# Optimization experiments

Hardware: AMD Instinct MI355X
Metric: run time of the kernel (lower is better)

## Reference

```python
import jax, jax.numpy as jnp
import numpy as np

B, P, OBS = 65536, 3, 48      # batch, players, per-player obs dim
N_PROP, N_EXT = 9, 2          # 9 prop encoders, players-1 = 2 teammate encoders
TEAM_OPP = 18 + 6 * N_EXT     # = 30; opponent slice starts here
OPP = OBS - TEAM_OPP          # = 18
ACT_DIM = 3
EXT_OUT = 576 // N_EXT        # = 288
ACT_LIMIT = 1.0
NEG_SLOPE = 0.01              # torch LeakyReLU default


def setup_inputs() -> dict:
    key = jax.random.key(0)
    ks = iter(jax.random.split(key, 32))
    r = lambda shape: jax.random.normal(next(ks), shape, jnp.float32) * 0.05
    return {
        "obs": jax.random.normal(next(ks), (B, P, OBS), jnp.float32),
        # 9 propEncoders per player: [2 -> 32 -> 64]
        "prop_W1": r((P, N_PROP, 2, 32)),  "prop_b1": r((P, N_PROP, 32)),
        "prop_W2": r((P, N_PROP, 32, 64)), "prop_b2": r((P, N_PROP, 64)),
        # 2 extEncoders per player: [6 -> 32 -> 288]
        "ext_W1": r((P, N_EXT, 6, 32)),       "ext_b1": r((P, N_EXT, 32)),
        "ext_W2": r((P, N_EXT, 32, EXT_OUT)), "ext_b2": r((P, N_EXT, EXT_OUT)),
        # oppEncoder per player: [18 -> 32 -> 576]
        "opp_W1": r((P, OPP, 32)),  "opp_b1": r((P, 32)),
        "opp_W2": r((P, 32, 576)),  "opp_b2": r((P, 576)),
        # pi head per player: [576 -> 256 -> 256 -> act_dim], LeakyReLU, Tanh out
        "pi_W1": r((P, 576, 256)),     "pi_b1": r((P, 256)),
        "pi_W2": r((P, 256, 256)),     "pi_b2": r((P, 256)),
        "pi_W3": r((P, 256, ACT_DIM)), "pi_b3": r((P, ACT_DIM)),
    }


def reference(obs, prop_W1, prop_b1, prop_W2, prop_b2,
              ext_W1, ext_b1, ext_W2, ext_b2,
              opp_W1, opp_b1, opp_W2, opp_b2,
              pi_W1, pi_b1, pi_W2, pi_b2, pi_W3, pi_b3):
    lrelu = lambda x: jax.nn.leaky_relu(x, NEG_SLOPE)
    b = obs.shape[0]

    # --- prop encoders: 9 tiny MLPs on 2-wide slices, batched via einsum ---
    o_prop = obs[:, :, :2 * N_PROP].reshape(b, P, N_PROP, 2)
    h = lrelu(jnp.einsum('bpni,pnio->bpno', o_prop, prop_W1) + prop_b1)
    h = lrelu(jnp.einsum('bpni,pnio->bpno', h, prop_W2) + prop_b2)  # [B,P,9,64]
    enc = h.reshape(b, P, 9 * 64)  # concat over the 9 encoders -> [B,P,576]

    # --- ext encoders: n_players-1 MLPs on 6-wide slices ---
    o_ext = obs[:, :, 18:TEAM_OPP].reshape(b, P, N_EXT, 6)
    e = lrelu(jnp.einsum('bpni,pnio->bpno', o_ext, ext_W1) + ext_b1)
    e = lrelu(jnp.einsum('bpni,pnio->bpno', e, ext_W2) + ext_b2)    # [B,P,2,288]
    enc = enc + e.reshape(b, P, 576)

    # --- opp encoder on the remaining slice ---
    o_opp = obs[:, :, TEAM_OPP:]
    z = lrelu(jnp.einsum('bpi,pio->bpo', o_opp, opp_W1) + opp_b1)
    z = lrelu(jnp.einsum('bpi,pio->bpo', z, opp_W2) + opp_b2)       # [B,P,576]
    enc = enc + z

    # --- actor head: 576 -> 256 -> 256 -> act_dim, tanh * act_limit ---
    h1 = lrelu(jnp.einsum('bpi,pio->bpo', enc, pi_W1) + pi_b1)
    h2 = lrelu(jnp.einsum('bpi,pio->bpo', h1, pi_W2) + pi_b2)
    out = jnp.tanh(jnp.einsum('bpi,pio->bpo', h2, pi_W3) + pi_b3)
    return ACT_LIMIT * out  # [B, P, act_dim]
```

## Files before the change

kernel.cpp:

```cpp
#include <hip/hip_runtime.h>
#include <math.h>


#define NEG_SLOPE 0.01f

#define OFF_B1A  0
#define OFF_ENCB 9216
#define OFF_PW1  175104
#define OFF_PW2  617472
#define OFF_PW3  814080
#define WS_TOTAL 826368

#define TILE_ENCB 18
#define TILE_PW1  342
#define TILE_PW2  1206
#define TILE_PW3  1590
#define TILE_END  1614

#define OBS_STRIDE 48
#define HS_STRIDE  104
#define ENC_STRIDE 200
#define H_STRIDE   264

typedef short bf16x8 __attribute__((ext_vector_type(8)));
typedef float f32x4  __attribute__((ext_vector_type(4)));
typedef float f32x2  __attribute__((ext_vector_type(2)));

__device__ __forceinline__ float lrelu(float x) { return fmaxf(x, NEG_SLOPE * x); }

__device__ __forceinline__ float u2f(unsigned int u) {
  union { unsigned int u; float f; } c; c.u = u; return c.f;
}

__device__ __forceinline__ unsigned int pk2bf(float a, float b) {
  union { float f; unsigned int u; } ca, cb; ca.f = a; cb.f = b;
  return __builtin_amdgcn_perm(cb.u + 0x8000u, ca.u + 0x8000u, 0x07060302u);
}

__device__ __forceinline__ unsigned short f2bf(float x) {
  union { float f; unsigned int u; } c; c.f = x;
  unsigned int u = (c.u + 0x7fffu + ((c.u >> 16) & 1u)) >> 16;
  return (unsigned short)u;
}

__global__ __launch_bounds__(256) void prep_kernel(
    const float* __restrict__ propW2, const float* __restrict__ extW1,
    const float* __restrict__ extW2,  const float* __restrict__ oppW1,
    const float* __restrict__ oppW2,  const float* __restrict__ piW1,
    const float* __restrict__ piW2,   const float* __restrict__ piW3,
    unsigned short* __restrict__ ws16)
{
  const int u = blockIdx.x * 256 + threadIdx.x;
  if (u >= (WS_TOTAL >> 3)) return;
  const int lane = u & 63;
  const int t = u >> 6;
  const int lm = lane & 15;
  const int kbase = (lane >> 4) << 3;

  unsigned short o8[8];

  if (t < TILE_ENCB) {
    int s = t;
    const int nt2 = s & 1; s >>= 1;
    const int go = s % 3; const int p = s / 3;
    const int n = go * 32 + nt2 * 16 + lm;
    #pragma unroll
    for (int j = 0; j < 8; ++j) {
      const int d = 16 + kbase + j;
      float v;
      if (n < 64) {
        const int g = n >> 5, o = n & 31, i = d - 18 - 6 * g;
        v = (i >= 0 && i < 6) ? extW1[((p * 2 + g) * 6 + i) * 32 + o] : 0.f;
      } else {
        const int o = n - 64, i = d - 30;
        v = (i >= 0) ? oppW1[(p * 18 + i) * 32 + o] : 0.f;
      }
      o8[j] = f2bf(v);
    }
  } else if (t < TILE_PW1) {
    int s = t - TILE_ENCB;
    const int nt2 = s & 1; s >>= 1;
    const int br = s % 3; s /= 3;
    const int kt = s % 18; const int p = s / 18;
    const int n = kt * 32 + nt2 * 16 + lm;
    #pragma unroll
    for (int j = 0; j < 8; ++j) {
      const int k_pos = kbase + j;
      const int kperm = (k_pos & 1) * 16 + (k_pos >> 1);
      float v;
      if (br == 0)      { const int g = kt >> 1;   v = propW2[((p*9+g)*32 + k_pos)*64 + (n - g*64)]; }
      else if (br == 1) { const int g = (kt >= 9); v = extW2 [((p*2+g)*32 + kperm)*288 + (n - g*288)]; }
      else              {                          v = oppW2 [(p*32 + kperm)*576 + n]; }
      o8[j] = f2bf(v);
    }
  } else if (t < TILE_PW2) {
    int s = t - TILE_PW1;
    const int nt = s & 15; s >>= 4;
    const int kt = s % 18; const int p = s / 18;
    const int col = nt * 16 + lm;
    #pragma unroll
    for (int j = 0; j < 8; ++j) {
      const int k_pos = kbase + j;
      const int kperm = (k_pos & 1) * 16 + (k_pos >> 1);
      o8[j] = f2bf(piW1[(p * 576 + kt * 32 + kperm) * 256 + col]);
    }
  } else if (t < TILE_PW3) {
    int s = t - TILE_PW2;
    const int nt = s & 15; s >>= 4;
    const int kt = s & 7; const int p = s >> 3;
    const int col = nt * 16 + lm;
    #pragma unroll
    for (int j = 0; j < 8; ++j) {
      const int k_pos = kbase + j;
      const int kperm = (k_pos & 1) * 16 + (k_pos >> 1);
      o8[j] = f2bf(piW2[(p * 256 + kt * 32 + kperm) * 256 + col]);
    }
  } else {
    int s = t - TILE_PW3;
    const int kt = s & 7; const int p = s >> 3;
    #pragma unroll
    for (int j = 0; j < 8; ++j) {
      const int k_pos = kbase + j;
      const int kperm = (k_pos & 1) * 16 + (k_pos >> 1);
      o8[j] = (lm < 3) ? f2bf(piW3[(p * 256 + kt * 32 + kperm) * 3 + lm]) : (unsigned short)0;
    }
  }

  *(uint4*)&ws16[(size_t)u * 8] = *(const uint4*)o8;
}

__global__ __launch_bounds__(256, 3) void fused_kernel(
    const float* __restrict__ obs,
    const float* __restrict__ propW1, const float* __restrict__ propB1,
    const float* __restrict__ propB2,
    const float* __restrict__ extB1,  const float* __restrict__ extB2,
    const float* __restrict__ oppB1,  const float* __restrict__ oppB2,
    const unsigned short* __restrict__ wsAll,
    const float* __restrict__ b1v, const float* __restrict__ b2v,
    const float* __restrict__ b3v,
    float* __restrict__ out)
{
  __shared__ __align__(16) unsigned short obs_s[64 * OBS_STRIDE];
  __shared__ __align__(16) unsigned short Hs[64 * HS_STRIDE];
  __shared__ __align__(16) unsigned short hbuf[64 * H_STRIDE];

  const unsigned short* b1aW = wsAll + OFF_B1A;
  const unsigned short* encB = wsAll + OFF_ENCB;
  const unsigned short* w1sw = wsAll + OFF_PW1;
  const unsigned short* w2sw = wsAll + OFF_PW2;
  const unsigned short* w3sw = wsAll + OFF_PW3;

  const int tid = threadIdx.x;
  const int p = blockIdx.y, brow = blockIdx.x;
  const int sbase = brow * 64;
  const int wv = tid >> 6, l = tid & 63, lm = l & 15, q = l >> 4;
  const f32x4 zz = {0.f, 0.f, 0.f, 0.f};

  {
    const int s = tid >> 2, c4 = tid & 3;
    if (c4 < 3) {
      const int c0 = c4 * 16;
      const float4* src = (const float4*)&obs[(sbase + s) * 144 + p * 48 + c0];
      float4 v0 = src[0], v1 = src[1], v2 = src[2], v3 = src[3];
      unsigned int pk[8];
      pk[0] = pk2bf(v0.x, v0.y); pk[1] = pk2bf(v0.z, v0.w);
      pk[2] = pk2bf(v1.x, v1.y); pk[3] = pk2bf(v1.z, v1.w);
      pk[4] = pk2bf(v2.x, v2.y); pk[5] = pk2bf(v2.z, v2.w);
      pk[6] = pk2bf(v3.x, v3.y); pk[7] = pk2bf(v3.z, v3.w);
      *(uint4*)&obs_s[s * OBS_STRIDE + c0]     = *(uint4*)&pk[0];
      *(uint4*)&obs_s[s * OBS_STRIDE + c0 + 8] = *(uint4*)&pk[4];
    }
  }
  __syncthreads();

  if (wv >= 1) {
    const int go = wv - 1;
    bf16x8 af[4];
    #pragma unroll
    for (int ms = 0; ms < 4; ++ms)
      af[ms] = *(const bf16x8*)&obs_s[(ms * 16 + lm) * OBS_STRIDE + 16 + q * 8];
    bf16x8 bf0 = *(const bf16x8*)&b1aW[((p * 3 + go) * 2 + 0) * 512 + l * 8];
    bf16x8 bf1 = *(const bf16x8*)&b1aW[((p * 3 + go) * 2 + 1) * 512 + l * 8];
    float bias0, bias1;
    if (go < 2) { bias0 = extB1[(p*2+go)*32 + lm]; bias1 = extB1[(p*2+go)*32 + 16 + lm]; }
    else        { bias0 = oppB1[p*32 + lm];        bias1 = oppB1[p*32 + 16 + lm]; }
    const f32x4 cb0 = {bias0, bias0, bias0, bias0};
    const f32x4 cb1 = {bias1, bias1, bias1, bias1};
    #pragma unroll
    for (int ms = 0; ms < 4; ++ms) {
      f32x4 c0 = __builtin_amdgcn_mfma_f32_16x16x32_bf16(af[ms], bf0, cb0, 0, 0, 0);
      f32x4 c1 = __builtin_amdgcn_mfma_f32_16x16x32_bf16(af[ms], bf1, cb1, 0, 0, 0);
      #pragma unroll
      for (int r = 0; r < 4; ++r) {
        unsigned int w = pk2bf(lrelu(c0[r]), lrelu(c1[r]));
        *(unsigned int*)&Hs[(ms * 16 + q * 4 + r) * HS_STRIDE + go * 32 + lm * 2] = w;
      }
    }
  }
  __syncthreads();

  float b1r[4];
  #pragma unroll
  for (int nt = 0; nt < 4; ++nt) b1r[nt] = b1v[p * 256 + wv * 64 + nt * 16 + lm];
  f32x4 acc[4][4];
  #pragma unroll
  for (int a = 0; a < 4; ++a)
    #pragma unroll
    for (int b = 0; b < 4; ++b) {
      f32x4 cb = {b1r[b], b1r[b], b1r[b], b1r[b]};
      acc[a][b] = cb;
    }

  for (int g = 0; g < 3; ++g) {
    int kts[2]; int nkt = 1;
    kts[0] = g * 6 + wv;
    if ((g & 1) == 0 && wv < 2)       { kts[1] = g * 6 + 4 + wv;       nkt = 2; }
    else if ((g & 1) == 1 && wv >= 2) { kts[1] = g * 6 + 4 + (wv - 2); nkt = 2; }

    for (int ik = 0; ik < nkt; ++ik) {
      const int kt = kts[ik], ktloc = kt - g * 6;
      const int gp = kt >> 1, ge = (kt >= 9) ? 1 : 0;

      bf16x8 apf[4];
      {
        f32x2 w0v[4], w1v[4], bbv[4];
        const float4* p4 = (const float4*)&propW1[(p * 9 + gp) * 64];
        float4 t0a = p4[q * 2],     t0b = p4[q * 2 + 1];
        float4 t1a = p4[8 + q * 2], t1b = p4[8 + q * 2 + 1];
        const float4* pb4 = (const float4*)&propB1[(p * 9 + gp) * 32];
        float4 tba = pb4[q * 2],    tbb = pb4[q * 2 + 1];
        w0v[0] = (f32x2){t0a.x, t0a.y}; w0v[1] = (f32x2){t0a.z, t0a.w};
        w0v[2] = (f32x2){t0b.x, t0b.y}; w0v[3] = (f32x2){t0b.z, t0b.w};
        w1v[0] = (f32x2){t1a.x, t1a.y}; w1v[1] = (f32x2){t1a.z, t1a.w};
        w1v[2] = (f32x2){t1b.x, t1b.y}; w1v[3] = (f32x2){t1b.z, t1b.w};
        bbv[0] = (f32x2){tba.x, tba.y}; bbv[1] = (f32x2){tba.z, tba.w};
        bbv[2] = (f32x2){tbb.x, tbb.y}; bbv[3] = (f32x2){tbb.z, tbb.w};
        #pragma unroll
        for (int ms = 0; ms < 4; ++ms) {
          const int row = ms * 16 + lm;
          const unsigned int xu = *(const unsigned int*)&obs_s[row * OBS_STRIDE + 2 * gp];
          const f32x2 x0v = {u2f(xu << 16), u2f(xu << 16)};
          const f32x2 x1v = {u2f(xu & 0xffff0000u), u2f(xu & 0xffff0000u)};
          unsigned int au[4];
          #pragma unroll
          for (int jj = 0; jj < 4; ++jj) {
            f32x2 h = bbv[jj] + x0v * w0v[jj] + x1v * w1v[jj];
            h = __builtin_elementwise_max(h, h * NEG_SLOPE);
            au[jj] = pk2bf(h.x, h.y);
          }
          __builtin_memcpy(&apf[ms], au, 16);
        }
      }

      const int ebase = (p * 18 + kt) * 6;
      bf16x8 wpf[2], wef[2], wof[2];
      float bp[2], be[2], bo[2];
      #pragma unroll
      for (int nt2 = 0; nt2 < 2; ++nt2) {
        wpf[nt2] = *(const bf16x8*)&encB[(ebase + nt2) * 512 + l * 8];
        wef[nt2] = *(const bf16x8*)&encB[(ebase + 2 + nt2) * 512 + l * 8];
        wof[nt2] = *(const bf16x8*)&encB[(ebase + 4 + nt2) * 512 + l * 8];
        const int nc = nt2 * 16 + lm;
        bp[nt2] = propB2[(p * 9 + gp) * 64 + (kt & 1) * 32 + nc];
        be[nt2] = extB2[(p * 2 + ge) * 288 + (kt - ge * 9) * 32 + nc];
        bo[nt2] = oppB2[p * 576 + kt * 32 + nc];
      }

      #pragma unroll
      for (int ms = 0; ms < 4; ++ms) {
        const int row = ms * 16 + lm;
        bf16x8 ae = *(const bf16x8*)&Hs[row * HS_STRIDE + ge * 32 + q * 8];
        bf16x8 ao = *(const bf16x8*)&Hs[row * HS_STRIDE + 64 + q * 8];
        float v0[4], v1[4];
        {
          f32x4 cp = __builtin_amdgcn_mfma_f32_16x16x32_bf16(apf[ms], wpf[0], zz, 0, 0, 0);
          f32x4 ce = __builtin_amdgcn_mfma_f32_16x16x32_bf16(ae,      wef[0], zz, 0, 0, 0);
          f32x4 co = __builtin_amdgcn_mfma_f32_16x16x32_bf16(ao,      wof[0], zz, 0, 0, 0);
          #pragma unroll
          for (int r = 0; r < 4; ++r)
            v0[r] = lrelu(cp[r] + bp[0]) + lrelu(ce[r] + be[0]) + lrelu(co[r] + bo[0]);
        }
        {
          f32x4 cp = __builtin_amdgcn_mfma_f32_16x16x32_bf16(apf[ms], wpf[1], zz, 0, 0, 0);
          f32x4 ce = __builtin_amdgcn_mfma_f32_16x16x32_bf16(ae,      wef[1], zz, 0, 0, 0);
          f32x4 co = __builtin_amdgcn_mfma_f32_16x16x32_bf16(ao,      wof[1], zz, 0, 0, 0);
          #pragma unroll
          for (int r = 0; r < 4; ++r)
            v1[r] = lrelu(cp[r] + bp[1]) + lrelu(ce[r] + be[1]) + lrelu(co[r] + bo[1]);
        }
        #pragma unroll
        for (int r = 0; r < 4; ++r)
          *(unsigned int*)&hbuf[(ms * 16 + q * 4 + r) * ENC_STRIDE + ktloc * 32 + lm * 2] =
              pk2bf(v0[r], v1[r]);
      }
    }
    __syncthreads();

    for (int ktloc = 0; ktloc < 6; ++ktloc) {
      const int kt = g * 6 + ktloc;
      bf16x8 afr[4], bfr[4];
      #pragma unroll
      for (int ms = 0; ms < 4; ++ms)
        afr[ms] = *(const bf16x8*)&hbuf[(ms * 16 + lm) * ENC_STRIDE + ktloc * 32 + q * 8];
      const int wb = ((p * 18 + kt) * 16 + wv * 4) * 512 + l * 8;
      #pragma unroll
      for (int nt = 0; nt < 4; ++nt)
        bfr[nt] = *(const bf16x8*)&w1sw[wb + nt * 512];
      #pragma unroll
      for (int ms = 0; ms < 4; ++ms)
        #pragma unroll
        for (int nt = 0; nt < 4; ++nt)
          acc[ms][nt] = __builtin_amdgcn_mfma_f32_16x16x32_bf16(afr[ms], bfr[nt], acc[ms][nt], 0, 0, 0);
    }
    __syncthreads();
  }

  #pragma unroll
  for (int ms = 0; ms < 4; ++ms)
    #pragma unroll
    for (int pi2 = 0; pi2 < 2; ++pi2)
      #pragma unroll
      for (int r = 0; r < 4; ++r) {
        float v0 = lrelu(acc[ms][pi2 * 2][r]);
        float v1 = lrelu(acc[ms][pi2 * 2 + 1][r]);
        *(unsigned int*)&hbuf[(ms * 16 + q * 4 + r) * H_STRIDE + (wv * 2 + pi2) * 32 + lm * 2] =
            pk2bf(v0, v1);
      }
  __syncthreads();

  {
    float b2r[4];
    #pragma unroll
    for (int nt = 0; nt < 4; ++nt) b2r[nt] = b2v[p * 256 + wv * 64 + nt * 16 + lm];
    #pragma unroll
    for (int a = 0; a < 4; ++a)
      #pragma unroll
      for (int b = 0; b < 4; ++b) {
        f32x4 cb = {b2r[b], b2r[b], b2r[b], b2r[b]};
        acc[a][b] = cb;
      }
  }
  for (int kt = 0; kt < 8; ++kt) {
    bf16x8 afr[4], bfr[4];
    #pragma unroll
    for (int ms = 0; ms < 4; ++ms)
      afr[ms] = *(const bf16x8*)&hbuf[(ms * 16 + lm) * H_STRIDE + kt * 32 + q * 8];
    const int wb = ((p * 8 + kt) * 16 + wv * 4) * 512 + l * 8;
    #pragma unroll
    for (int nt = 0; nt < 4; ++nt)
      bfr[nt] = *(const bf16x8*)&w2sw[wb + nt * 512];
    #pragma unroll
    for (int ms = 0; ms < 4; ++ms)
      #pragma unroll
      for (int nt = 0; nt < 4; ++nt)
        acc[ms][nt] = __builtin_amdgcn_mfma_f32_16x16x32_bf16(afr[ms], bfr[nt], acc[ms][nt], 0, 0, 0);
  }
  __syncthreads();
  #pragma unroll
  for (int ms = 0; ms < 4; ++ms)
    #pragma unroll
    for (int pi2 = 0; pi2 < 2; ++pi2)
      #pragma unroll
      for (int r = 0; r < 4; ++r) {
        float v0 = lrelu(acc[ms][pi2 * 2][r]);
        float v1 = lrelu(acc[ms][pi2 * 2 + 1][r]);
        *(unsigned int*)&hbuf[(ms * 16 + q * 4 + r) * H_STRIDE + (wv * 2 + pi2) * 32 + lm * 2] =
            pk2bf(v0, v1);
      }
  __syncthreads();

  const float bias3 = (lm < 3) ? b3v[p * 3 + lm] : 0.f;
  f32x4 a3 = {bias3, bias3, bias3, bias3};
  for (int kt = 0; kt < 8; ++kt) {
    bf16x8 afr = *(const bf16x8*)&hbuf[(wv * 16 + lm) * H_STRIDE + kt * 32 + q * 8];
    bf16x8 bfr = *(const bf16x8*)&w3sw[((p * 8 + kt) * 64 + l) * 8];
    a3 = __builtin_amdgcn_mfma_f32_16x16x32_bf16(afr, bfr, a3, 0, 0, 0);
  }
  if (lm < 3) {
    #pragma unroll
    for (int r = 0; r < 4; ++r) {
      const int s = wv * 16 + q * 4 + r;
      out[(sbase + s) * 9 + p * 3 + lm] = tanhf(a3[r]);
    }
  }
}

extern "C" void kernel_launch(void* const* d_in, const int* in_sizes, int n_in,
                              void* d_out, int out_size, void* d_ws, size_t ws_size,
                              hipStream_t stream)
{
  (void)in_sizes; (void)n_in; (void)out_size; (void)ws_size;
  const float* obs    = (const float*)d_in[0];
  const float* propW1 = (const float*)d_in[1];
  const float* propB1 = (const float*)d_in[2];
  const float* propW2 = (const float*)d_in[3];
  const float* propB2 = (const float*)d_in[4];
  const float* extW1  = (const float*)d_in[5];
  const float* extB1  = (const float*)d_in[6];
  const float* extW2  = (const float*)d_in[7];
  const float* extB2  = (const float*)d_in[8];
  const float* oppW1  = (const float*)d_in[9];
  const float* oppB1  = (const float*)d_in[10];
  const float* oppW2  = (const float*)d_in[11];
  const float* oppB2  = (const float*)d_in[12];
  const float* piW1   = (const float*)d_in[13];
  const float* piB1   = (const float*)d_in[14];
  const float* piW2   = (const float*)d_in[15];
  const float* piB2   = (const float*)d_in[16];
  const float* piW3   = (const float*)d_in[17];
  const float* piB3   = (const float*)d_in[18];
  float* out = (float*)d_out;
  unsigned short* ws16 = (unsigned short*)d_ws;

  prep_kernel<<<dim3(((WS_TOTAL >> 3) + 255) / 256), dim3(256), 0, stream>>>(
      propW2, extW1, extW2, oppW1, oppW2, piW1, piW2, piW3, ws16);

  fused_kernel<<<dim3(65536 / 64, 3), dim3(256), 0, stream>>>(
      obs, propW1, propB1, propB2, extB1, extB2, oppB1, oppB2,
      ws16, piB1, piB2, piB3, out);
}
```

Measured before the change: 245.9 us.

## Double threads per block to eight waves splitting GEMM N-tiles

```diff
diff --git a/kernel.cpp b/kernel.cpp
--- a/kernel.cpp
+++ b/kernel.cpp
@@ -15,7 +15,6 @@
 #define TILE_PW1  342
 #define TILE_PW2  1206
 #define TILE_PW3  1590
-#define TILE_END  1614
 
 #define OBS_STRIDE 48
 #define HS_STRIDE  104
@@ -27,6 +26,11 @@
 typedef float f32x2  __attribute__((ext_vector_type(2)));
 
 __device__ __forceinline__ float lrelu(float x) { return fmaxf(x, NEG_SLOPE * x); }
+
+__device__ __forceinline__ f32x4 lrelu4(f32x4 x) {
+  return __builtin_elementwise_max(x, x * NEG_SLOPE);
+}
+__device__ __forceinline__ f32x4 splat4(float b) { return (f32x4){b, b, b, b}; }
 
 __device__ __forceinline__ float u2f(unsigned int u) {
   union { unsigned int u; float f; } c; c.u = u; return c.f;
@@ -129,7 +133,7 @@
   *(uint4*)&ws16[(size_t)u * 8] = *(const uint4*)o8;
 }
 
-__global__ __launch_bounds__(256, 3) void fused_kernel(
+__global__ __launch_bounds__(512, 6) void fused_kernel(
     const float* __restrict__ obs,
     const float* __restrict__ propW1, const float* __restrict__ propB1,
     const float* __restrict__ propB2,
@@ -156,7 +160,7 @@
   const int wv = tid >> 6, l = tid & 63, lm = l & 15, q = l >> 4;
   const f32x4 zz = {0.f, 0.f, 0.f, 0.f};
 
-  {
+  if (tid < 256) {
     const int s = tid >> 2, c4 = tid & 3;
     if (c4 < 3) {
       const int c0 = c4 * 16;
@@ -173,7 +177,7 @@
   }
   __syncthreads();
 
-  if (wv >= 1) {
+  if (wv >= 1 && wv <= 3) {
     const int go = wv - 1;
     bf16x8 af[4];
     #pragma unroll
@@ -184,41 +188,32 @@
     float bias0, bias1;
     if (go < 2) { bias0 = extB1[(p*2+go)*32 + lm]; bias1 = extB1[(p*2+go)*32 + 16 + lm]; }
     else        { bias0 = oppB1[p*32 + lm];        bias1 = oppB1[p*32 + 16 + lm]; }
-    const f32x4 cb0 = {bias0, bias0, bias0, bias0};
-    const f32x4 cb1 = {bias1, bias1, bias1, bias1};
+    const f32x4 cb0 = splat4(bias0), cb1 = splat4(bias1);
     #pragma unroll
     for (int ms = 0; ms < 4; ++ms) {
-      f32x4 c0 = __builtin_amdgcn_mfma_f32_16x16x32_bf16(af[ms], bf0, cb0, 0, 0, 0);
-      f32x4 c1 = __builtin_amdgcn_mfma_f32_16x16x32_bf16(af[ms], bf1, cb1, 0, 0, 0);
-      #pragma unroll
-      for (int r = 0; r < 4; ++r) {
-        unsigned int w = pk2bf(lrelu(c0[r]), lrelu(c1[r]));
-        *(unsigned int*)&Hs[(ms * 16 + q * 4 + r) * HS_STRIDE + go * 32 + lm * 2] = w;
-      }
+      f32x4 c0 = lrelu4(__builtin_amdgcn_mfma_f32_16x16x32_bf16(af[ms], bf0, cb0, 0, 0, 0));
+      f32x4 c1 = lrelu4(__builtin_amdgcn_mfma_f32_16x16x32_bf16(af[ms], bf1, cb1, 0, 0, 0));
+      #pragma unroll
+      for (int r = 0; r < 4; ++r)
+        *(unsigned int*)&Hs[(ms * 16 + q * 4 + r) * HS_STRIDE + go * 32 + lm * 2] =
+            pk2bf(c0[r], c1[r]);
     }
   }
   __syncthreads();
 
-  float b1r[4];
+  float b1r[2];
   #pragma unroll
-  for (int nt = 0; nt < 4; ++nt) b1r[nt] = b1v[p * 256 + wv * 64 + nt * 16 + lm];
-  f32x4 acc[4][4];
+  for (int nt = 0; nt < 2; ++nt) b1r[nt] = b1v[p * 256 + wv * 32 + nt * 16 + lm];
+  f32x4 acc[4][2];
   #pragma unroll
-  for (int a = 0; a < 4; ++a)
-    #pragma unroll
-    for (int b = 0; b < 4; ++b) {
-      f32x4 cb = {b1r[b], b1r[b], b1r[b], b1r[b]};
-      acc[a][b] = cb;
-    }
+  for (int a = 0; a < 4; ++a) {
+    acc[a][0] = splat4(b1r[0]);
+    acc[a][1] = splat4(b1r[1]);
+  }
 
   for (int g = 0; g < 3; ++g) {
-    int kts[2]; int nkt = 1;
-    kts[0] = g * 6 + wv;
-    if ((g & 1) == 0 && wv < 2)       { kts[1] = g * 6 + 4 + wv;       nkt = 2; }
-    else if ((g & 1) == 1 && wv >= 2) { kts[1] = g * 6 + 4 + (wv - 2); nkt = 2; }
-
-    for (int ik = 0; ik < nkt; ++ik) {
-      const int kt = kts[ik], ktloc = kt - g * 6;
+    if (wv < 6) {
+      const int kt = g * 6 + wv, ktloc = wv;
       const int gp = kt >> 1, ge = (kt >= 9) ? 1 : 0;
 
       bf16x8 apf[4];
@@ -271,116 +266,105 @@
         const int row = ms * 16 + lm;
         bf16x8 ae = *(const bf16x8*)&Hs[row * HS_STRIDE + ge * 32 + q * 8];
         bf16x8 ao = *(const bf16x8*)&Hs[row * HS_STRIDE + 64 + q * 8];
-        float v0[4], v1[4];
+        f32x4 s0, s1;
         {
           f32x4 cp = __builtin_amdgcn_mfma_f32_16x16x32_bf16(apf[ms], wpf[0], zz, 0, 0, 0);
           f32x4 ce = __builtin_amdgcn_mfma_f32_16x16x32_bf16(ae,      wef[0], zz, 0, 0, 0);
           f32x4 co = __builtin_amdgcn_mfma_f32_16x16x32_bf16(ao,      wof[0], zz, 0, 0, 0);
-          #pragma unroll
-          for (int r = 0; r < 4; ++r)
-            v0[r] = lrelu(cp[r] + bp[0]) + lrelu(ce[r] + be[0]) + lrelu(co[r] + bo[0]);
+          s0 = lrelu4(cp + splat4(bp[0])) + lrelu4(ce + splat4(be[0])) + lrelu4(co + splat4(bo[0]));
         }
         {
           f32x4 cp = __builtin_amdgcn_mfma_f32_16x16x32_bf16(apf[ms], wpf[1], zz, 0, 0, 0);
           f32x4 ce = __builtin_amdgcn_mfma_f32_16x16x32_bf16(ae,      wef[1], zz, 0, 0, 0);
           f32x4 co = __builtin_amdgcn_mfma_f32_16x16x32_bf16(ao,      wof[1], zz, 0, 0, 0);
-          #pragma unroll
-          for (int r = 0; r < 4; ++r)
-            v1[r] = lrelu(cp[r] + bp[1]) + lrelu(ce[r] + be[1]) + lrelu(co[r] + bo[1]);
+          s1 = lrelu4(cp + splat4(bp[1])) + lrelu4(ce + splat4(be[1])) + lrelu4(co + splat4(bo[1]));
         }
         #pragma unroll
         for (int r = 0; r < 4; ++r)
           *(unsigned int*)&hbuf[(ms * 16 + q * 4 + r) * ENC_STRIDE + ktloc * 32 + lm * 2] =
-              pk2bf(v0[r], v1[r]);
+              pk2bf(s0[r], s1[r]);
       }
     }
     __syncthreads();
 
     for (int ktloc = 0; ktloc < 6; ++ktloc) {
       const int kt = g * 6 + ktloc;
-      bf16x8 afr[4], bfr[4];
+      bf16x8 afr[4], bfr[2];
       #pragma unroll
       for (int ms = 0; ms < 4; ++ms)
         afr[ms] = *(const bf16x8*)&hbuf[(ms * 16 + lm) * ENC_STRIDE + ktloc * 32 + q * 8];
-      const int wb = ((p * 18 + kt) * 16 + wv * 4) * 512 + l * 8;
-      #pragma unroll
-      for (int nt = 0; nt < 4; ++nt)
-        bfr[nt] = *(const bf16x8*)&w1sw[wb + nt * 512];
-      #pragma unroll
-      for (int ms = 0; ms < 4; ++ms)
-        #pragma unroll
-        for (int nt = 0; nt < 4; ++nt)
-          acc[ms][nt] = __builtin_amdgcn_mfma_f32_16x16x32_bf16(afr[ms], bfr[nt], acc[ms][nt], 0, 0, 0);
+      const int wb = ((p * 18 + kt) * 16 + wv * 2) * 512 + l * 8;
+      bfr[0] = *(const bf16x8*)&w1sw[wb];
+      bfr[1] = *(const bf16x8*)&w1sw[wb + 512];
+      #pragma unroll
+      for (int ms = 0; ms < 4; ++ms) {
+        acc[ms][0] = __builtin_amdgcn_mfma_f32_16x16x32_bf16(afr[ms], bfr[0], acc[ms][0], 0, 0, 0);
+        acc[ms][1] = __builtin_amdgcn_mfma_f32_16x16x32_bf16(afr[ms], bfr[1], acc[ms][1], 0, 0, 0);
+      }
     }
     __syncthreads();
   }
 
   #pragma unroll
-  for (int ms = 0; ms < 4; ++ms)
-    #pragma unroll
-    for (int pi2 = 0; pi2 < 2; ++pi2)
-      #pragma unroll
-      for (int r = 0; r < 4; ++r) {
-        float v0 = lrelu(acc[ms][pi2 * 2][r]);
-        float v1 = lrelu(acc[ms][pi2 * 2 + 1][r]);
-        *(unsigned int*)&hbuf[(ms * 16 + q * 4 + r) * H_STRIDE + (wv * 2 + pi2) * 32 + lm * 2] =
-            pk2bf(v0, v1);
-      }
+  for (int ms = 0; ms < 4; ++ms) {
+    f32x4 a0 = lrelu4(acc[ms][0]);
+    f32x4 a1 = lrelu4(acc[ms][1]);
+    #pragma unroll
+    for (int r = 0; r < 4; ++r)
+      *(unsigned int*)&hbuf[(ms * 16 + q * 4 + r) * H_STRIDE + wv * 32 + lm * 2] =
+          pk2bf(a0[r], a1[r]);
+  }
   __syncthreads();
 
   {
-    float b2r[4];
-    #pragma unroll
-    for (int nt = 0; nt < 4; ++nt) b2r[nt] = b2v[p * 256 + wv * 64 + nt * 16 + lm];
-    #pragma unroll
-    for (int a = 0; a < 4; ++a)
-      #pragma unroll
-      for (int b = 0; b < 4; ++b) {
-        f32x4 cb = {b2r[b], b2r[b], b2r[b], b2r[b]};
-        acc[a][b] = cb;
-      }
+    float b2r0 = b2v[p * 256 + wv * 32 + lm];
+    float b2r1 = b2v[p * 256 + wv * 32 + 16 + lm];
+    #pragma unroll
+    for (int a = 0; a < 4; ++a) {
+      acc[a][0] = splat4(b2r0);
+      acc[a][1] = splat4(b2r1);
+    }
   }
   for (int kt = 0; kt < 8; ++kt) {
-    bf16x8 afr[4], bfr[4];
+    bf16x8 afr[4], bfr[2];
     #pragma unroll
     for (int ms = 0; ms < 4; ++ms)
       afr[ms] = *(const bf16x8*)&hbuf[(ms * 16 + lm) * H_STRIDE + kt * 32 + q * 8];
-    const int wb = ((p * 8 + kt) * 16 + wv * 4) * 512 + l * 8;
-    #pragma unroll
-    for (int nt = 0; nt < 4; ++nt)
-      bfr[nt] = *(const bf16x8*)&w2sw[wb + nt * 512];
-    #pragma unroll
-    for (int ms = 0; ms < 4; ++ms)
-      #pragma unroll
-      for (int nt = 0; nt < 4; ++nt)
-        acc[ms][nt] = __builtin_amdgcn_mfma_f32_16x16x32_bf16(afr[ms], bfr[nt], acc[ms][nt], 0, 0, 0);
+    const int wb = ((p * 8 + kt) * 16 + wv * 2) * 512 + l * 8;
+    bfr[0] = *(const bf16x8*)&w2sw[wb];
+    bfr[1] = *(const bf16x8*)&w2sw[wb + 512];
+    #pragma unroll
+    for (int ms = 0; ms < 4; ++ms) {
+      acc[ms][0] = __builtin_amdgcn_mfma_f32_16x16x32_bf16(afr[ms], bfr[0], acc[ms][0], 0, 0, 0);
+      acc[ms][1] = __builtin_amdgcn_mfma_f32_16x16x32_bf16(afr[ms], bfr[1], acc[ms][1], 0, 0, 0);
+    }
   }
   __syncthreads();
   #pragma unroll
-  for (int ms = 0; ms < 4; ++ms)
-    #pragma unroll
-    for (int pi2 = 0; pi2 < 2; ++pi2)
+  for (int ms = 0; ms < 4; ++ms) {
+    f32x4 a0 = lrelu4(acc[ms][0]);
+    f32x4 a1 = lrelu4(acc[ms][1]);
+    #pragma unroll
+    for (int r = 0; r < 4; ++r)
+      *(unsigned int*)&hbuf[(ms * 16 + q * 4 + r) * H_STRIDE + wv * 32 + lm * 2] =
+          pk2bf(a0[r], a1[r]);
+  }
+  __syncthreads();
+
+  if (wv < 4) {
+    const float bias3 = (lm < 3) ? b3v[p * 3 + lm] : 0.f;
+    f32x4 a3 = splat4(bias3);
+    for (int kt = 0; kt < 8; ++kt) {
+      bf16x8 afr = *(const bf16x8*)&hbuf[(wv * 16 + lm) * H_STRIDE + kt * 32 + q * 8];
+      bf16x8 bfr = *(const bf16x8*)&w3sw[((p * 8 + kt) * 64 + l) * 8];
+      a3 = __builtin_amdgcn_mfma_f32_16x16x32_bf16(afr, bfr, a3, 0, 0, 0);
+    }
+    if (lm < 3) {
       #pragma unroll
       for (int r = 0; r < 4; ++r) {
-        float v0 = lrelu(acc[ms][pi2 * 2][r]);
-        float v1 = lrelu(acc[ms][pi2 * 2 + 1][r]);
-        *(unsigned int*)&hbuf[(ms * 16 + q * 4 + r) * H_STRIDE + (wv * 2 + pi2) * 32 + lm * 2] =
-            pk2bf(v0, v1);
-      }
-  __syncthreads();
-
-  const float bias3 = (lm < 3) ? b3v[p * 3 + lm] : 0.f;
-  f32x4 a3 = {bias3, bias3, bias3, bias3};
-  for (int kt = 0; kt < 8; ++kt) {
-    bf16x8 afr = *(const bf16x8*)&hbuf[(wv * 16 + lm) * H_STRIDE + kt * 32 + q * 8];
-    bf16x8 bfr = *(const bf16x8*)&w3sw[((p * 8 + kt) * 64 + l) * 8];
-    a3 = __builtin_amdgcn_mfma_f32_16x16x32_bf16(afr, bfr, a3, 0, 0, 0);
-  }
-  if (lm < 3) {
-    #pragma unroll
-    for (int r = 0; r < 4; ++r) {
-      const int s = wv * 16 + q * 4 + r;
-      out[(sbase + s) * 9 + p * 3 + lm] = tanhf(a3[r]);
+        const int s = wv * 16 + q * 4 + r;
+        out[(sbase + s) * 9 + p * 3 + lm] = tanhf(a3[r]);
+      }
     }
   }
 }
@@ -415,7 +399,7 @@
   prep_kernel<<<dim3(((WS_TOTAL >> 3) + 255) / 256), dim3(256), 0, stream>>>(
       propW2, extW1, extW2, oppW1, oppW2, piW1, piW2, piW3, ws16);
 
-  fused_kernel<<<dim3(65536 / 64, 3), dim3(256), 0, stream>>>(
+  fused_kernel<<<dim3(65536 / 64, 3), dim3(512), 0, stream>>>(
       obs, propW1, propB1, propB2, extB1, extB2, oppB1, oppB2,
       ws16, piB1, piB2, piB3, out);
 }
```

New measurement: 426.2 us. 1.73x slower.

## Alias shared buffers, rebalance encoder k-tile groups, raise occupancy to four blocks

Applied to the files above, without the earlier changes.

```diff
diff --git a/kernel.cpp b/kernel.cpp
--- a/kernel.cpp
+++ b/kernel.cpp
@@ -15,12 +15,15 @@
 #define TILE_PW1  342
 #define TILE_PW2  1206
 #define TILE_PW3  1590
-#define TILE_END  1614
 
 #define OBS_STRIDE 48
 #define HS_STRIDE  104
-#define ENC_STRIDE 200
+#define ENC_STRIDE 136
 #define H_STRIDE   264
+
+#define SM_OBS 8704
+#define SM_HS  11776
+#define SM_TOT 18432
 
 typedef short bf16x8 __attribute__((ext_vector_type(8)));
 typedef float f32x4  __attribute__((ext_vector_type(4)));
@@ -28,8 +31,19 @@
 
 __device__ __forceinline__ float lrelu(float x) { return fmaxf(x, NEG_SLOPE * x); }
 
+__device__ __forceinline__ f32x4 lrelu4(f32x4 x) {
+  return __builtin_elementwise_max(x, x * NEG_SLOPE);
+}
+__device__ __forceinline__ f32x4 splat4(float b) { return (f32x4){b, b, b, b}; }
+
 __device__ __forceinline__ float u2f(unsigned int u) {
   union { unsigned int u; float f; } c; c.u = u; return c.f;
+}
+
+__device__ __forceinline__ float fast_tanh(float x) {
+  x = fminf(15.f, fmaxf(-15.f, x));
+  float e = __expf(2.f * x);
+  return (e - 1.f) / (e + 1.f);
 }
 
 __device__ __forceinline__ unsigned int pk2bf(float a, float b) {
@@ -129,7 +143,7 @@
   *(uint4*)&ws16[(size_t)u * 8] = *(const uint4*)o8;
 }
 
-__global__ __launch_bounds__(256, 3) void fused_kernel(
+__global__ __launch_bounds__(256, 4) void fused_kernel(
     const float* __restrict__ obs,
     const float* __restrict__ propW1, const float* __restrict__ propB1,
     const float* __restrict__ propB2,
@@ -140,9 +154,11 @@
     const float* __restrict__ b3v,
     float* __restrict__ out)
 {
-  __shared__ __align__(16) unsigned short obs_s[64 * OBS_STRIDE];
-  __shared__ __align__(16) unsigned short Hs[64 * HS_STRIDE];
-  __shared__ __align__(16) unsigned short hbuf[64 * H_STRIDE];
+  __shared__ __align__(16) unsigned short smem[SM_TOT];
+  unsigned short* encb  = smem;
+  unsigned short* obs_s = smem + SM_OBS;
+  unsigned short* Hsb   = smem + SM_HS;
+  unsigned short* hbuf  = smem;
 
   const unsigned short* b1aW = wsAll + OFF_B1A;
   const unsigned short* encB = wsAll + OFF_ENCB;
@@ -184,17 +200,15 @@
     float bias0, bias1;
     if (go < 2) { bias0 = extB1[(p*2+go)*32 + lm]; bias1 = extB1[(p*2+go)*32 + 16 + lm]; }
     else        { bias0 = oppB1[p*32 + lm];        bias1 = oppB1[p*32 + 16 + lm]; }
-    const f32x4 cb0 = {bias0, bias0, bias0, bias0};
-    const f32x4 cb1 = {bias1, bias1, bias1, bias1};
+    const f32x4 cb0 = splat4(bias0), cb1 = splat4(bias1);
     #pragma unroll
     for (int ms = 0; ms < 4; ++ms) {
-      f32x4 c0 = __builtin_amdgcn_mfma_f32_16x16x32_bf16(af[ms], bf0, cb0, 0, 0, 0);
-      f32x4 c1 = __builtin_amdgcn_mfma_f32_16x16x32_bf16(af[ms], bf1, cb1, 0, 0, 0);
-      #pragma unroll
-      for (int r = 0; r < 4; ++r) {
-        unsigned int w = pk2bf(lrelu(c0[r]), lrelu(c1[r]));
-        *(unsigned int*)&Hs[(ms * 16 + q * 4 + r) * HS_STRIDE + go * 32 + lm * 2] = w;
-      }
+      f32x4 c0 = lrelu4(__builtin_amdgcn_mfma_f32_16x16x32_bf16(af[ms], bf0, cb0, 0, 0, 0));
+      f32x4 c1 = lrelu4(__builtin_amdgcn_mfma_f32_16x16x32_bf16(af[ms], bf1, cb1, 0, 0, 0));
+      #pragma unroll
+      for (int r = 0; r < 4; ++r)
+        *(unsigned int*)&Hsb[(ms * 16 + q * 4 + r) * HS_STRIDE + go * 32 + lm * 2] =
+            pk2bf(c0[r], c1[r]);
     }
   }
   __syncthreads();
@@ -206,19 +220,12 @@
   #pragma unroll
   for (int a = 0; a < 4; ++a)
     #pragma unroll
-    for (int b = 0; b < 4; ++b) {
-      f32x4 cb = {b1r[b], b1r[b], b1r[b], b1r[b]};
-      acc[a][b] = cb;
-    }
-
-  for (int g = 0; g < 3; ++g) {
-    int kts[2]; int nkt = 1;
-    kts[0] = g * 6 + wv;
-    if ((g & 1) == 0 && wv < 2)       { kts[1] = g * 6 + 4 + wv;       nkt = 2; }
-    else if ((g & 1) == 1 && wv >= 2) { kts[1] = g * 6 + 4 + (wv - 2); nkt = 2; }
-
-    for (int ik = 0; ik < nkt; ++ik) {
-      const int kt = kts[ik], ktloc = kt - g * 6;
+    for (int b = 0; b < 4; ++b) acc[a][b] = splat4(b1r[b]);
+
+  for (int g = 0; g < 5; ++g) {
+    const int nk = (g < 4) ? 4 : 2;
+    if (wv < nk) {
+      const int kt = g * 4 + wv, ktloc = wv;
       const int gp = kt >> 1, ge = (kt >= 9) ? 1 : 0;
 
       bf16x8 apf[4];
@@ -269,39 +276,35 @@
       #pragma unroll
       for (int ms = 0; ms < 4; ++ms) {
         const int row = ms * 16 + lm;
-        bf16x8 ae = *(const bf16x8*)&Hs[row * HS_STRIDE + ge * 32 + q * 8];
-        bf16x8 ao = *(const bf16x8*)&Hs[row * HS_STRIDE + 64 + q * 8];
-        float v0[4], v1[4];
+        bf16x8 ae = *(const bf16x8*)&Hsb[row * HS_STRIDE + ge * 32 + q * 8];
+        bf16x8 ao = *(const bf16x8*)&Hsb[row * HS_STRIDE + 64 + q * 8];
+        f32x4 s0, s1;
         {
           f32x4 cp = __builtin_amdgcn_mfma_f32_16x16x32_bf16(apf[ms], wpf[0], zz, 0, 0, 0);
           f32x4 ce = __builtin_amdgcn_mfma_f32_16x16x32_bf16(ae,      wef[0], zz, 0, 0, 0);
           f32x4 co = __builtin_amdgcn_mfma_f32_16x16x32_bf16(ao,      wof[0], zz, 0, 0, 0);
-          #pragma unroll
-          for (int r = 0; r < 4; ++r)
-            v0[r] = lrelu(cp[r] + bp[0]) + lrelu(ce[r] + be[0]) + lrelu(co[r] + bo[0]);
+          s0 = lrelu4(cp + splat4(bp[0])) + lrelu4(ce + splat4(be[0])) + lrelu4(co + splat4(bo[0]));
         }
         {
           f32x4 cp = __builtin_amdgcn_mfma_f32_16x16x32_bf16(apf[ms], wpf[1], zz, 0, 0, 0);
           f32x4 ce = __builtin_amdgcn_mfma_f32_16x16x32_bf16(ae,      wef[1], zz, 0, 0, 0);
           f32x4 co = __builtin_amdgcn_mfma_f32_16x16x32_bf16(ao,      wof[1], zz, 0, 0, 0);
-          #pragma unroll
-          for (int r = 0; r < 4; ++r)
-            v1[r] = lrelu(cp[r] + bp[1]) + lrelu(ce[r] + be[1]) + lrelu(co[r] + bo[1]);
+          s1 = lrelu4(cp + splat4(bp[1])) + lrelu4(ce + splat4(be[1])) + lrelu4(co + splat4(bo[1]));
         }
         #pragma unroll
         for (int r = 0; r < 4; ++r)
-          *(unsigned int*)&hbuf[(ms * 16 + q * 4 + r) * ENC_STRIDE + ktloc * 32 + lm * 2] =
-              pk2bf(v0[r], v1[r]);
+          *(unsigned int*)&encb[(ms * 16 + q * 4 + r) * ENC_STRIDE + ktloc * 32 + lm * 2] =
+              pk2bf(s0[r], s1[r]);
       }
     }
     __syncthreads();
 
-    for (int ktloc = 0; ktloc < 6; ++ktloc) {
-      const int kt = g * 6 + ktloc;
+    for (int ktloc = 0; ktloc < nk; ++ktloc) {
+      const int kt = g * 4 + ktloc;
       bf16x8 afr[4], bfr[4];
       #pragma unroll
       for (int ms = 0; ms < 4; ++ms)
-        afr[ms] = *(const bf16x8*)&hbuf[(ms * 16 + lm) * ENC_STRIDE + ktloc * 32 + q * 8];
+        afr[ms] = *(const bf16x8*)&encb[(ms * 16 + lm) * ENC_STRIDE + ktloc * 32 + q * 8];
       const int wb = ((p * 18 + kt) * 16 + wv * 4) * 512 + l * 8;
       #pragma unroll
       for (int nt = 0; nt < 4; ++nt)
@@ -318,14 +321,14 @@
   #pragma unroll
   for (int ms = 0; ms < 4; ++ms)
     #pragma unroll
-    for (int pi2 = 0; pi2 < 2; ++pi2)
-      #pragma unroll
-      for (int r = 0; r < 4; ++r) {
-        float v0 = lrelu(acc[ms][pi2 * 2][r]);
-        float v1 = lrelu(acc[ms][pi2 * 2 + 1][r]);
+    for (int pi2 = 0; pi2 < 2; ++pi2) {
+      f32x4 a0 = lrelu4(acc[ms][pi2 * 2]);
+      f32x4 a1 = lrelu4(acc[ms][pi2 * 2 + 1]);
+      #pragma unroll
+      for (int r = 0; r < 4; ++r)
         *(unsigned int*)&hbuf[(ms * 16 + q * 4 + r) * H_STRIDE + (wv * 2 + pi2) * 32 + lm * 2] =
-            pk2bf(v0, v1);
-      }
+            pk2bf(a0[r], a1[r]);
+    }
   __syncthreads();
 
   {
@@ -335,10 +338,7 @@
     #pragma unroll
     for (int a = 0; a < 4; ++a)
       #pragma unroll
-      for (int b = 0; b < 4; ++b) {
-        f32x4 cb = {b2r[b], b2r[b], b2r[b], b2r[b]};
-        acc[a][b] = cb;
-      }
+      for (int b = 0; b < 4; ++b) acc[a][b] = splat4(b2r[b]);
   }
   for (int kt = 0; kt < 8; ++kt) {
     bf16x8 afr[4], bfr[4];
@@ -359,18 +359,18 @@
   #pragma unroll
   for (int ms = 0; ms < 4; ++ms)
     #pragma unroll
-    for (int pi2 = 0; pi2 < 2; ++pi2)
-      #pragma unroll
-      for (int r = 0; r < 4; ++r) {
-        float v0 = lrelu(acc[ms][pi2 * 2][r]);
-        float v1 = lrelu(acc[ms][pi2 * 2 + 1][r]);
+    for (int pi2 = 0; pi2 < 2; ++pi2) {
+      f32x4 a0 = lrelu4(acc[ms][pi2 * 2]);
+      f32x4 a1 = lrelu4(acc[ms][pi2 * 2 + 1]);
+      #pragma unroll
+      for (int r = 0; r < 4; ++r)
         *(unsigned int*)&hbuf[(ms * 16 + q * 4 + r) * H_STRIDE + (wv * 2 + pi2) * 32 + lm * 2] =
-            pk2bf(v0, v1);
-      }
+            pk2bf(a0[r], a1[r]);
+    }
   __syncthreads();
 
   const float bias3 = (lm < 3) ? b3v[p * 3 + lm] : 0.f;
-  f32x4 a3 = {bias3, bias3, bias3, bias3};
+  f32x4 a3 = splat4(bias3);
   for (int kt = 0; kt < 8; ++kt) {
     bf16x8 afr = *(const bf16x8*)&hbuf[(wv * 16 + lm) * H_STRIDE + kt * 32 + q * 8];
     bf16x8 bfr = *(const bf16x8*)&w3sw[((p * 8 + kt) * 64 + l) * 8];
@@ -380,7 +380,7 @@
     #pragma unroll
     for (int r = 0; r < 4; ++r) {
       const int s = wv * 16 + q * 4 + r;
-      out[(sbase + s) * 9 + p * 3 + lm] = tanhf(a3[r]);
+      out[(sbase + s) * 9 + p * 3 + lm] = fast_tanh(a3[r]);
     }
   }
 }
```

Measured after the change: 307.0 us. +24.8%, slower.
